# Performance work log

Measured on AMD Instinct MI355X. Metric: run time of the kernel, lower is better.

The kernel has to match this reference:

```python
import jax, jax.numpy as jnp
import numpy as np

PATCH = 7
STACK = 16
TUBE = 2
IMG = 84
EMBED = 1024
GH = IMG // PATCH   # 12
GW = IMG // PATCH   # 12
GD = STACK // TUBE  # 8
PF = 1 * PATCH * PATCH  # per-frame patch feature (C*p*p) = 49


def _sincos_1d(dim, pos):
    # pos: [N] -> [N, dim]
    omega = 1.0 / (10000.0 ** (np.arange(dim // 2, dtype=np.float64) / (dim / 2.0)))
    out = pos[:, None].astype(np.float64) * omega[None, :]
    return np.concatenate([np.sin(out), np.cos(out)], axis=1)


def get_3d_sincos_pos_embed(grid_h, grid_w, grid_depth, embed_dim):
    # standard video sincos split: 1/4 temporal, 3/4 spatial (half h, half w)
    dim_t = embed_dim // 4
    dim_s = embed_dim - dim_t
    emb_t = _sincos_1d(dim_t, np.arange(grid_depth))            # [D, dim_t]
    emb_h = _sincos_1d(dim_s // 2, np.arange(grid_h))           # [gh, dim_s/2]
    emb_w = _sincos_1d(dim_s - dim_s // 2, np.arange(grid_w))   # [gw, ...]
    # spatial tokens row-major (h major, w minor), matching unfold ordering
    emb_hw = np.concatenate(
        [np.repeat(emb_h, grid_w, axis=0), np.tile(emb_w, (grid_h, 1))], axis=1
    )  # [gh*gw, dim_s]
    ns = grid_h * grid_w
    # token order: depth major, spatial minor (matches D*Ns reshape in forward)
    pe = np.concatenate(
        [np.repeat(emb_t, ns, axis=0), np.tile(emb_hw, (grid_depth, 1))], axis=1
    )  # [D*Ns, embed_dim]
    return pe.astype(np.float32)


def setup_inputs() -> dict:
    key = jax.random.key(0)
    k1, k2, k3 = jax.random.split(key, 3)
    B = 64
    video = jax.random.normal(k1, (B, STACK, 1, IMG, IMG), dtype=jnp.float32)
    tubelet_in = TUBE * PF  # 98
    W = jax.random.normal(k2, (EMBED, tubelet_in), dtype=jnp.float32) * (tubelet_in ** -0.5)
    b = jax.random.normal(k3, (EMBED,), dtype=jnp.float32) * 0.02
    pos_embed = jnp.asarray(get_3d_sincos_pos_embed(GH, GW, GD, EMBED))[None]  # [1, N, E]
    return {"video": video, "W": W, "b": b, "pos_embed": pos_embed}


def reference(video, W, b, pos_embed):
    B, T, C, H, W_ = video.shape
    p = PATCH
    gh, gw = H // p, W_ // p
    ns = gh * gw
    # extract_tensor_patches (stride == window, no padding): pure reshape/transpose
    x = video.reshape(B * T, C, gh, p, gw, p)
    x = x.transpose(0, 2, 4, 1, 3, 5)                 # [BT, gh, gw, C, p, p]
    x = x.reshape(B, T, ns, C * p * p)                # [B, T, Ns, Pf]
    x = x.reshape(B, GD, TUBE, ns, C * p * p)
    x = x.transpose(0, 1, 3, 2, 4)                    # [B, D, Ns, Ts, Pf]
    tubelets = x.reshape(B, GD * ns, TUBE * C * p * p)  # [B, N, 98]
    tokens = jnp.einsum("bnk,ek->bne", tubelets, W) + b + pos_embed
    return tokens
```

## Files before the change

kernel.cpp:

```cpp
#include <hip/hip_runtime.h>
#include <hip/hip_bf16.h>
#include <stdint.h>


typedef __bf16 bf16_t;
typedef bf16_t bf16x8 __attribute__((ext_vector_type(8)));
typedef float f32x4 __attribute__((ext_vector_type(4)));

#define B_      64
#define N_TOK   1152
#define M_TOT   (B_ * N_TOK)
#define E_      1024
#define KP      128
#define K_REAL  98
#define BM      128
#define BN      128
#define MT_N    (M_TOT / BM)
#define NT_N    (E_ / BN)

__global__ void wconv_kernel(const float* __restrict__ W, bf16_t* __restrict__ Wb) {
    int idx = blockIdx.x * 256 + threadIdx.x;
    int k = idx & (KP - 1);
    int e = idx >> 7;
    float v = (k < K_REAL) ? W[e * K_REAL + k] : 0.f;
    Wb[e * KP + (k ^ ((e & 7) << 3))] = (bf16_t)v;
}

__global__ void im2col_kernel(const float* __restrict__ video, bf16_t* __restrict__ A) {
    int idx = blockIdx.x * 256 + threadIdx.x;
    int g = idx & 15;
    int m = idx >> 4;
    int b  = m / N_TOK;
    int n  = m - b * N_TOK;
    int d  = n / 144, s = n - d * 144;
    int i  = s / 12,  jj = s - i * 12;
    const float* base = video + (b * 16 + d * 2) * 7056 + (i * 7) * 84 + jj * 7;
    bf16_t vals[8];
#pragma unroll
    for (int j = 0; j < 8; ++j) {
        int k = g * 8 + j;
        float v = 0.f;
        if (k < K_REAL) {
            int ts = (k >= 49) ? 1 : 0;
            int f  = k - ts * 49;
            int fy = f / 7, fx = f - fy * 7;
            v = base[ts * 7056 + fy * 84 + fx];
        }
        vals[j] = (bf16_t)v;
    }
    int col = (g * 8) ^ ((m & 7) << 3);
    *(bf16x8*)&A[(long)m * KP + col] = *(const bf16x8*)vals;
}

__global__ __launch_bounds__(256) void gemm_kernel(
    const bf16_t* __restrict__ A, const bf16_t* __restrict__ Wb,
    const float* __restrict__ bias, const float* __restrict__ pos,
    float* __restrict__ out) {
    __shared__ __align__(16) bf16_t As[BM * KP];
    __shared__ __align__(16) bf16_t Bs[BN * KP];

    const int tid  = threadIdx.x;
    const int wv   = tid >> 6;
    const int lane = tid & 63;

    const int bid = blockIdx.x;
    const int mt  = bid % MT_N;
    const int nt  = bid / MT_N;
    const long m0 = (long)mt * BM;
    const int  n0 = nt * BN;

    {
        const char* gA = (const char*)(A + m0 * KP);
        const char* gB = (const char*)(Wb + (long)n0 * KP);
        char* lA = (char*)As;
        char* lB = (char*)Bs;
#pragma unroll
        for (int i = 0; i < 8; ++i) {
            int off = (wv * 8 + i) * 1024;
            __builtin_amdgcn_global_load_lds(
                (const __attribute__((address_space(1))) void*)(gA + off + lane * 16),
                (__attribute__((address_space(3))) void*)(lA + off), 16, 0, 0);
        }
#pragma unroll
        for (int i = 0; i < 8; ++i) {
            int off = (wv * 8 + i) * 1024;
            __builtin_amdgcn_global_load_lds(
                (const __attribute__((address_space(1))) void*)(gB + off + lane * 16),
                (__attribute__((address_space(3))) void*)(lB + off), 16, 0, 0);
        }
    }
    __syncthreads();

    const int wr = wv >> 1, wc = wv & 1;
    const int lr = lane & 15;
    const int lk = (lane >> 4) * 8;
    const int xsw = (lr & 7) << 3;

    f32x4 acc[4][4];
#pragma unroll
    for (int mi = 0; mi < 4; ++mi)
#pragma unroll
        for (int ni = 0; ni < 4; ++ni)
            acc[mi][ni] = (f32x4){0.f, 0.f, 0.f, 0.f};

#pragma unroll
    for (int kk = 0; kk < 4; ++kk) {
        bf16x8 a[4], b[4];
        const int col = (kk * 32 + lk) ^ xsw;
#pragma unroll
        for (int mi = 0; mi < 4; ++mi)
            a[mi] = *(const bf16x8*)&As[(wr * 64 + mi * 16 + lr) * KP + col];
#pragma unroll
        for (int ni = 0; ni < 4; ++ni)
            b[ni] = *(const bf16x8*)&Bs[(wc * 64 + ni * 16 + lr) * KP + col];
#pragma unroll
        for (int mi = 0; mi < 4; ++mi)
#pragma unroll
            for (int ni = 0; ni < 4; ++ni)
                acc[mi][ni] = __builtin_amdgcn_mfma_f32_16x16x32_bf16(
                    a[mi], b[ni], acc[mi][ni], 0, 0, 0);
    }

    const int ntok_blk = (mt % 9) * BM;
    const int row4 = (lane >> 4) * 4;
#pragma unroll
    for (int ni = 0; ni < 4; ++ni) {
        const int e  = n0 + wc * 64 + ni * 16 + lr;
        const float be = bias[e];
#pragma unroll
        for (int mi = 0; mi < 4; ++mi) {
            const int mloc = wr * 64 + mi * 16 + row4;
            const long mg  = m0 + mloc;
            const int ntok = ntok_blk + mloc;
#pragma unroll
            for (int r = 0; r < 4; ++r) {
                float vout = acc[mi][ni][r] + be + pos[(ntok + r) * E_ + e];
                __builtin_nontemporal_store(vout, &out[(mg + r) * (long)E_ + e]);
            }
        }
    }
}

extern "C" void kernel_launch(void* const* d_in, const int* in_sizes, int n_in,
                              void* d_out, int out_size, void* d_ws, size_t ws_size,
                              hipStream_t stream) {
    const float* video = (const float*)d_in[0];
    const float* W     = (const float*)d_in[1];
    const float* bias  = (const float*)d_in[2];
    const float* pos   = (const float*)d_in[3];
    float* out = (float*)d_out;

    bf16_t* A_ws = (bf16_t*)d_ws;
    bf16_t* W_ws = (bf16_t*)((char*)d_ws + (size_t)M_TOT * KP * 2);

    wconv_kernel<<<(E_ * KP) / 256, 256, 0, stream>>>(W, W_ws);
    im2col_kernel<<<(M_TOT * 16) / 256, 256, 0, stream>>>(video, A_ws);
    gemm_kernel<<<MT_N * NT_N, 256, 0, stream>>>(A_ws, W_ws, bias, pos, out);
}
```

Baseline: 443.9 us.

## Fuse im2col into GEMM, swap MFMA operands for vectorized stores, reorder block mapping

Removes the separate im2col kernel and its bf16 workspace round-trip: each GEMM block now gathers its tubelet patches straight from the video into LDS. The MFMA operands are swapped so that each lane's accumulator holds four consecutive embedding columns, which allows 16-byte vector loads of bias and pos and 16-byte nontemporal stores of the output. Block indexing now puts the 8 N-tiles of an M-tile on adjacent blocks, so their redundant video gathers can hit in L2. The cost is that the same patch data is gathered and converted 8 times, once per N-tile, inside the GEMM.

```diff
diff --git a/kernel.cpp b/kernel.cpp
--- a/kernel.cpp
+++ b/kernel.cpp
@@ -26,34 +26,8 @@
     Wb[e * KP + (k ^ ((e & 7) << 3))] = (bf16_t)v;
 }
 
-__global__ void im2col_kernel(const float* __restrict__ video, bf16_t* __restrict__ A) {
-    int idx = blockIdx.x * 256 + threadIdx.x;
-    int g = idx & 15;
-    int m = idx >> 4;
-    int b  = m / N_TOK;
-    int n  = m - b * N_TOK;
-    int d  = n / 144, s = n - d * 144;
-    int i  = s / 12,  jj = s - i * 12;
-    const float* base = video + (b * 16 + d * 2) * 7056 + (i * 7) * 84 + jj * 7;
-    bf16_t vals[8];
-#pragma unroll
-    for (int j = 0; j < 8; ++j) {
-        int k = g * 8 + j;
-        float v = 0.f;
-        if (k < K_REAL) {
-            int ts = (k >= 49) ? 1 : 0;
-            int f  = k - ts * 49;
-            int fy = f / 7, fx = f - fy * 7;
-            v = base[ts * 7056 + fy * 84 + fx];
-        }
-        vals[j] = (bf16_t)v;
-    }
-    int col = (g * 8) ^ ((m & 7) << 3);
-    *(bf16x8*)&A[(long)m * KP + col] = *(const bf16x8*)vals;
-}
-
 __global__ __launch_bounds__(256) void gemm_kernel(
-    const bf16_t* __restrict__ A, const bf16_t* __restrict__ Wb,
+    const float* __restrict__ video, const bf16_t* __restrict__ Wb,
     const float* __restrict__ bias, const float* __restrict__ pos,
     float* __restrict__ out) {
     __shared__ __align__(16) bf16_t As[BM * KP];
@@ -64,23 +38,16 @@
     const int lane = tid & 63;
 
     const int bid = blockIdx.x;
-    const int mt  = bid % MT_N;
-    const int nt  = bid / MT_N;
+    const int nt  = bid & 7;
+    const int mt  = bid >> 3;
     const long m0 = (long)mt * BM;
     const int  n0 = nt * BN;
+    const int  bb = mt / 9;
+    const int  ntok_blk = (mt - bb * 9) * BM;
 
     {
-        const char* gA = (const char*)(A + m0 * KP);
         const char* gB = (const char*)(Wb + (long)n0 * KP);
-        char* lA = (char*)As;
         char* lB = (char*)Bs;
-#pragma unroll
-        for (int i = 0; i < 8; ++i) {
-            int off = (wv * 8 + i) * 1024;
-            __builtin_amdgcn_global_load_lds(
-                (const __attribute__((address_space(1))) void*)(gA + off + lane * 16),
-                (__attribute__((address_space(3))) void*)(lA + off), 16, 0, 0);
-        }
 #pragma unroll
         for (int i = 0; i < 8; ++i) {
             int off = (wv * 8 + i) * 1024;
@@ -89,54 +56,79 @@
                 (__attribute__((address_space(3))) void*)(lB + off), 16, 0, 0);
         }
     }
+
+    {
+        const float* vbase = video + (size_t)(bb * 16) * 7056;
+#pragma unroll
+        for (int it = 0; it < 8; ++it) {
+            int gi    = it * 256 + tid;
+            int m_loc = gi >> 4;
+            int g     = gi & 15;
+            int n  = ntok_blk + m_loc;
+            int d  = n / 144, s = n - d * 144;
+            int i  = s / 12,  jj = s - i * 12;
+            const float* fbase = vbase + (size_t)(d * 2) * 7056 + (i * 7) * 84 + jj * 7;
+            bf16_t vals[8];
+#pragma unroll
+            for (int u = 0; u < 8; ++u) {
+                int k = g * 8 + u;
+                float v = 0.f;
+                if (k < K_REAL) {
+                    int ts = (k >= 49) ? 1 : 0;
+                    int f  = k - ts * 49;
+                    int fy = f / 7, fx = f - fy * 7;
+                    v = fbase[ts * 7056 + fy * 84 + fx];
+                }
+                vals[u] = (bf16_t)v;
+            }
+            int col = (g * 8) ^ ((m_loc & 7) << 3);
+            *(bf16x8*)&As[m_loc * KP + col] = *(const bf16x8*)vals;
+        }
+    }
     __syncthreads();
 
-    const int wr = wv >> 1, wc = wv & 1;
+    const int we = wv >> 1, wt = wv & 1;
     const int lr = lane & 15;
     const int lk = (lane >> 4) * 8;
     const int xsw = (lr & 7) << 3;
 
     f32x4 acc[4][4];
 #pragma unroll
-    for (int mi = 0; mi < 4; ++mi)
+    for (int ei = 0; ei < 4; ++ei)
 #pragma unroll
-        for (int ni = 0; ni < 4; ++ni)
-            acc[mi][ni] = (f32x4){0.f, 0.f, 0.f, 0.f};
+        for (int ti = 0; ti < 4; ++ti)
+            acc[ei][ti] = (f32x4){0.f, 0.f, 0.f, 0.f};
 
 #pragma unroll
     for (int kk = 0; kk < 4; ++kk) {
         bf16x8 a[4], b[4];
         const int col = (kk * 32 + lk) ^ xsw;
 #pragma unroll
-        for (int mi = 0; mi < 4; ++mi)
-            a[mi] = *(const bf16x8*)&As[(wr * 64 + mi * 16 + lr) * KP + col];
+        for (int ei = 0; ei < 4; ++ei)
+            a[ei] = *(const bf16x8*)&Bs[(we * 64 + ei * 16 + lr) * KP + col];
 #pragma unroll
-        for (int ni = 0; ni < 4; ++ni)
-            b[ni] = *(const bf16x8*)&Bs[(wc * 64 + ni * 16 + lr) * KP + col];
+        for (int ti = 0; ti < 4; ++ti)
+            b[ti] = *(const bf16x8*)&As[(wt * 64 + ti * 16 + lr) * KP + col];
 #pragma unroll
-        for (int mi = 0; mi < 4; ++mi)
+        for (int ei = 0; ei < 4; ++ei)
 #pragma unroll
-            for (int ni = 0; ni < 4; ++ni)
-                acc[mi][ni] = __builtin_amdgcn_mfma_f32_16x16x32_bf16(
-                    a[mi], b[ni], acc[mi][ni], 0, 0, 0);
+            for (int ti = 0; ti < 4; ++ti)
+                acc[ei][ti] = __builtin_amdgcn_mfma_f32_16x16x32_bf16(
+                    a[ei], b[ti], acc[ei][ti], 0, 0, 0);
     }
 
-    const int ntok_blk = (mt % 9) * BM;
     const int row4 = (lane >> 4) * 4;
 #pragma unroll
-    for (int ni = 0; ni < 4; ++ni) {
-        const int e  = n0 + wc * 64 + ni * 16 + lr;
-        const float be = bias[e];
+    for (int ei = 0; ei < 4; ++ei) {
+        const int e_base = n0 + we * 64 + ei * 16 + row4;
+        const f32x4 bias4 = *(const f32x4*)&bias[e_base];
 #pragma unroll
-        for (int mi = 0; mi < 4; ++mi) {
-            const int mloc = wr * 64 + mi * 16 + row4;
-            const long mg  = m0 + mloc;
-            const int ntok = ntok_blk + mloc;
-#pragma unroll
-            for (int r = 0; r < 4; ++r) {
-                float vout = acc[mi][ni][r] + be + pos[(ntok + r) * E_ + e];
-                __builtin_nontemporal_store(vout, &out[(mg + r) * (long)E_ + e]);
-            }
+        for (int ti = 0; ti < 4; ++ti) {
+            const int tok = wt * 64 + ti * 16 + lr;
+            const f32x4 pos4 = *(const f32x4*)&pos[(ntok_blk + tok) * E_ + e_base];
+            f32x4 vout = acc[ei][ti] + bias4 + pos4;
+            __builtin_nontemporal_store(
+                vout, (f32x4*)&out[(m0 + tok) * (long)E_ + e_base]);
         }
     }
 }
@@ -150,10 +142,8 @@
     const float* pos   = (const float*)d_in[3];
     float* out = (float*)d_out;
 
-    bf16_t* A_ws = (bf16_t*)d_ws;
-    bf16_t* W_ws = (bf16_t*)((char*)d_ws + (size_t)M_TOT * KP * 2);
+    bf16_t* W_ws = (bf16_t*)d_ws;
 
     wconv_kernel<<<(E_ * KP) / 256, 256, 0, stream>>>(W, W_ws);
-    im2col_kernel<<<(M_TOT * 16) / 256, 256, 0, stream>>>(video, A_ws);
-    gemm_kernel<<<MT_N * NT_N, 256, 0, stream>>>(A_ws, W_ws, bias, pos, out);
+    gemm_kernel<<<MT_N * NT_N, 256, 0, stream>>>(video, W_ws, bias, pos, out);
 }
```

New measurement: 517.3 us. 16.5% more time.
